# Kernel tuning notes

Measured on AMD Instinct MI355X. Metric: run time of the kernel, lower is better.

The kernel has to match this reference:

```python
import jax, jax.numpy as jnp
import numpy as np

B, T, D, H, L = 32, 512, 256, 512, 3


def setup_inputs() -> dict:
    key = jax.random.key(0)
    ks = jax.random.split(key, 14)
    def lin(k, fan_in, shape):
        return jax.random.normal(k, shape, jnp.float32) / np.sqrt(fan_in)
    inp = {"x": jax.random.normal(ks[0], (B, T, D), jnp.float32)}
    dims_in = [D, H, H]
    i = 1
    for l in range(L):
        inp[f"Wi{l}"] = lin(ks[i + 0], dims_in[l], (3 * H, dims_in[l]))
        inp[f"bi{l}"] = lin(ks[i + 1], dims_in[l], (3 * H,))
        inp[f"Wh{l}"] = lin(ks[i + 2], H, (3 * H, H))
        inp[f"bh{l}"] = lin(ks[i + 3], H, (3 * H,))
        i += 4
    return inp


def _cell(Wi, bi, Wh, bh, xin, h):
    # faithful to ExponentialGatingGRUCell (h2h term appears twice in n preact)
    h2h = h @ Wh.T + bh                      # [B, 3H]
    preact = xin @ Wi.T + bi + h2h           # [B, 3H]
    g = jax.nn.sigmoid(preact[:, : 2 * H])
    r, z = g[:, :H], g[:, H:]
    r = jnp.exp(-jnp.exp(-r))
    z = jnp.exp(-jnp.exp(-z))
    n = jnp.tanh(preact[:, 2 * H:] + r * h2h[:, 2 * H:])
    return (1.0 - z) * n + z * h


def _forward(x, params):
    h0 = tuple(jnp.zeros((x.shape[0], H), x.dtype) for _ in range(L))

    def step(carry, x_t):
        hs = list(carry)
        inp = x_t
        for l in range(L):
            Wi, bi, Wh, bh = params[l]
            hs[l] = _cell(Wi, bi, Wh, bh, inp, hs[l])
            inp = hs[l]
        return tuple(hs), None

    hT, _ = jax.lax.scan(step, h0, jnp.swapaxes(x, 0, 1))  # scan over time
    return hT[-1][:, None, :]  # [B, 1, H]


def reference(x, Wi0, bi0, Wh0, bh0, Wi1, bi1, Wh1, bh1, Wi2, bi2, Wh2, bh2):
    params = [(Wi0, bi0, Wh0, bh0), (Wi1, bi1, Wh1, bh1), (Wi2, bi2, Wh2, bh2)]
    return _forward(x, params)
```

## Files before the change

kernel.cpp:

```cpp
#include <hip/hip_runtime.h>
#include <hip/hip_bf16.h>

typedef __attribute__((ext_vector_type(4))) float fx4;
typedef __attribute__((ext_vector_type(8))) short bf8;
typedef __attribute__((ext_vector_type(4))) short sx4;
typedef __attribute__((ext_vector_type(4))) int ix4;

#define NBLK 96
#define HSZ (32 * 512)

__device__ __forceinline__ short f2bf(float f) {
  __hip_bfloat16 h = __float2bfloat16(f);
  return *reinterpret_cast<short*>(&h);
}
__device__ __forceinline__ float bf2f(short s) {
  union { unsigned u; float f; } c; c.u = ((unsigned)(unsigned short)s) << 16; return c.f;
}
__device__ __forceinline__ float rcpf(float x) { return __builtin_amdgcn_rcpf(x); }
__device__ __forceinline__ bf8 asbf8(ix4 v) { union { ix4 i; bf8 b; } u; u.i = v; return u.b; }

#define LDH(dst, p, OFF) \
  asm volatile("global_load_dwordx4 %0, %1, off offset:" OFF " sc0 sc1" \
               : "=v"(dst) : "v"(p) : "memory")
#define LDP(dst, p, OFF) \
  asm volatile("global_load_dwordx4 %0, %1, off offset:" OFF \
               : "=v"(dst) : "v"(p) : "memory")
#define LD8(OP, A, P) do { \
  OP(A[0], P, "0");   OP(A[1], P, "64");  OP(A[2], P, "128"); OP(A[3], P, "192"); \
  OP(A[4], P, "256"); OP(A[5], P, "320"); OP(A[6], P, "384"); OP(A[7], P, "448"); } while (0)
#define ST4_C(p, v) \
  asm volatile("global_store_dword %0, %1, off sc0 sc1" :: "v"(p), "v"(v) : "memory")
#define LD4_C(d, p) \
  asm volatile("global_load_dword %0, %1, off sc0 sc1\n\ts_waitcnt vmcnt(0)" \
               : "=v"(d) : "v"(p) : "memory")

__global__ __launch_bounds__(256) void conv_x_k(const float* __restrict__ x,
                                                short* __restrict__ xhi, short* __restrict__ xlo) {
  int i = blockIdx.x * 256 + threadIdx.x;
  fx4 v = *(const fx4*)(x + (size_t)i * 4);
  int k = (i * 4) & 255;
  int row = (i * 4) >> 8;
  int b = row >> 9, t = row & 511;
  sx4 hi, lo;
#pragma unroll
  for (int e = 0; e < 4; ++e) {
    hi[e] = f2bf(v[e]);
    lo[e] = f2bf(v[e] - bf2f(hi[e]));
  }
  size_t o = ((size_t)(t * 32 + b)) * 256 + k;
  *(sx4*)(xhi + o) = hi;
  *(sx4*)(xlo + o) = lo;
}

__device__ __forceinline__ void gate_wave(const int* flags, int base, int lane, int need) {
  const int* fp = flags + base + (lane & 31);
  while (true) {
    int v; LD4_C(v, fp);
    if (__ballot(v >= need) == ~0ull) break;
    __builtin_amdgcn_s_sleep(1);
  }
}

template<int L>
__device__ __forceinline__ void rec3_body(
    float (*m_lds)[32][52], float* bias_s,
    const short* __restrict__ xth, const short* __restrict__ xtl,
    const float* __restrict__ Wi, const float* __restrict__ bi,
    const float* __restrict__ Wh, const float* __restrict__ bh,
    short* __restrict__ hgl, const short* __restrict__ hgp,
    int* flags, float* __restrict__ out, int p)
{
  const int tid = threadIdx.x;
  const int j0 = p * 16;
  const int w = tid >> 6, lane = tid & 63, lm = lane & 15, lk = lane >> 4;
  const bool inW = (w < 2);
  constexpr int KIN = (L == 0) ? 256 : 512;

  const int kbase = inW ? ((L == 0) ? 0 : w * 256) : (w - 2) * 256;
  const float* Wf = inW ? Wi : Wh;
  const int wstr = inW ? KIN : 512;

  bf8 bwh[3][8], bwl[3][8];
#pragma unroll
  for (int g = 0; g < 3; ++g) {
    const int grow = g * 512 + j0 + lm;
#pragma unroll
    for (int ks = 0; ks < 8; ++ks) {
      const float* src = Wf + (size_t)grow * wstr + kbase + ks * 32 + lk * 8;
      fx4 f0 = *(const fx4*)(src);
      fx4 f1 = *(const fx4*)(src + 4);
      bf8 vh, vl;
#pragma unroll
      for (int e = 0; e < 4; ++e) {
        vh[e] = f2bf(f0[e]);     vl[e] = f2bf(f0[e] - bf2f(vh[e]));
        vh[4 + e] = f2bf(f1[e]); vl[4 + e] = f2bf(f1[e] - bf2f(vh[4 + e]));
      }
      bwh[g][ks] = vh; bwl[g][ks] = vl;
    }
  }
  if (tid < 48) bias_s[tid] = bi[(tid >> 4) * 512 + j0 + (tid & 15)];
  else if (tid < 96) {
    const int u = tid - 48;
    bias_s[48 + u] = bh[(u >> 4) * 512 + j0 + (u & 15)];
  }
  {
    const int zb = tid >> 3, zc = (tid & 7) * 2;
    ST4_C((int*)(hgl + (size_t)4 * HSZ + (size_t)zb * 512 + j0 + zc), 0);
    ST4_C((int*)(hgl + (size_t)5 * HSZ + (size_t)zb * 512 + j0 + zc), 0);
  }
  asm volatile("s_waitcnt vmcnt(0)" ::: "memory");
  __syncthreads();
  if (tid == 0) ST4_C(flags + L * 32 + p, 2);

  const int cb = tid >> 3, c2 = (tid & 7) * 2;
  float hv0 = 0.f, hv1 = 0.f;
  int bufw = 0;

  for (int s = 0; s < 512; ++s) {
    const int bufr = (bufw == 0) ? 2 : bufw - 1;
    ix4 rh[2][8], rl[2][8];
    if (L == 0 && inW) {
      const short* xh = xth + (size_t)(s * 32 + w * 16 + lm) * 256 + lk * 8;
      const short* xl = xtl + (size_t)(s * 32 + w * 16 + lm) * 256 + lk * 8;
      LD8(LDP, rh[0], xh);
      LD8(LDP, rl[0], xl);
    }

    if (!inW) {
      gate_wave(flags, L * 32, lane, s + 2);
    } else {
      if (L > 0) gate_wave(flags, (L - 1) * 32, lane, s + 3);
      if (L < 2) gate_wave(flags, (L + 1) * 32, lane, s);
    }

    if (inW) {
      if constexpr (L > 0) {
        const short* base = hgp + (size_t)(bufw * 2) * HSZ + (size_t)lm * 512 + kbase + lk * 8;
        LD8(LDH, rh[0], base);
        LD8(LDH, rh[1], base + 16 * 512);
        LD8(LDH, rl[0], base + HSZ);
        LD8(LDH, rl[1], base + HSZ + 16 * 512);
      }
    } else {
      const short* base = hgl + (size_t)(bufr * 2) * HSZ + (size_t)lm * 512 + kbase + lk * 8;
      LD8(LDH, rh[0], base);
      LD8(LDH, rh[1], base + 16 * 512);
      LD8(LDH, rl[0], base + HSZ);
      LD8(LDH, rl[1], base + HSZ + 16 * 512);
    }
    asm volatile("s_waitcnt vmcnt(0)" ::: "memory");
    __builtin_amdgcn_sched_barrier(0);

    fx4 acc[2][3];
#pragma unroll
    for (int mt = 0; mt < 2; ++mt)
#pragma unroll
      for (int g = 0; g < 3; ++g) acc[mt][g] = (fx4){0.f, 0.f, 0.f, 0.f};

    if (L == 0 && inW) {
#pragma unroll
      for (int ks = 0; ks < 8; ++ks) {
        bf8 ah = asbf8(rh[0][ks]);
        bf8 al = asbf8(rl[0][ks]);
#pragma unroll
        for (int g = 0; g < 3; ++g) {
          acc[0][g] = __builtin_amdgcn_mfma_f32_16x16x32_bf16(ah, bwh[g][ks], acc[0][g], 0, 0, 0);
          acc[0][g] = __builtin_amdgcn_mfma_f32_16x16x32_bf16(al, bwh[g][ks], acc[0][g], 0, 0, 0);
          acc[0][g] = __builtin_amdgcn_mfma_f32_16x16x32_bf16(ah, bwl[g][ks], acc[0][g], 0, 0, 0);
        }
      }
    } else {
#pragma unroll
      for (int ks = 0; ks < 8; ++ks) {
#pragma unroll
        for (int mt = 0; mt < 2; ++mt) {
          bf8 ah = asbf8(rh[mt][ks]);
          bf8 al = asbf8(rl[mt][ks]);
#pragma unroll
          for (int g = 0; g < 3; ++g) {
            acc[mt][g] = __builtin_amdgcn_mfma_f32_16x16x32_bf16(ah, bwh[g][ks], acc[mt][g], 0, 0, 0);
            acc[mt][g] = __builtin_amdgcn_mfma_f32_16x16x32_bf16(al, bwh[g][ks], acc[mt][g], 0, 0, 0);
            acc[mt][g] = __builtin_amdgcn_mfma_f32_16x16x32_bf16(ah, bwl[g][ks], acc[mt][g], 0, 0, 0);
          }
        }
      }
    }

    if (L == 0 && inW) {
#pragma unroll
      for (int g = 0; g < 3; ++g)
#pragma unroll
        for (int q = 0; q < 4; ++q)
          m_lds[0][w * 16 + lk * 4 + q][g * 16 + lm] = acc[0][g][q];
    } else {
#pragma unroll
      for (int mt = 0; mt < 2; ++mt)
#pragma unroll
        for (int g = 0; g < 3; ++g)
#pragma unroll
          for (int q = 0; q < 4; ++q)
            m_lds[w][mt * 16 + lk * 4 + q][g * 16 + lm] = acc[mt][g][q];
    }
    __syncthreads();

    float av[3][2], hh[3][2];
#pragma unroll
    for (int g = 0; g < 3; ++g)
#pragma unroll
      for (int e = 0; e < 2; ++e) {
        const int c = g * 16 + c2 + e;
        float ain = m_lds[0][cb][c];
        if (L > 0) ain += m_lds[1][cb][c];
        av[g][e] = ain + bias_s[c];
        hh[g][e] = m_lds[2][cb][c] + m_lds[3][cb][c] + bias_s[48 + c];
      }
    float hvv[2] = {hv0, hv1}, hn[2];
#pragma unroll
    for (int e = 0; e < 2; ++e) {
      float pr = av[0][e] + hh[0][e];
      float pz = av[1][e] + hh[1][e];
      float h2n = hh[2][e];
      float pn = av[2][e] + h2n;
      float sr = rcpf(1.f + __expf(-pr));
      float rr = __expf(-__expf(-sr));
      float sz = rcpf(1.f + __expf(-pz));
      float zz = __expf(-__expf(-sz));
      float na = pn + rr * h2n;
      float ex = __expf(2.f * na);
      float nn = 1.f - 2.f * rcpf(ex + 1.f);
      hn[e] = (1.f - zz) * nn + zz * hvv[e];
    }
    hv0 = hn[0]; hv1 = hn[1];
    short h0h = f2bf(hn[0]), h0l = f2bf(hn[0] - bf2f(h0h));
    short h1h = f2bf(hn[1]), h1l = f2bf(hn[1] - bf2f(h1h));
    int packh = (int)(unsigned short)h0h | ((int)(unsigned short)h1h << 16);
    int packl = (int)(unsigned short)h0l | ((int)(unsigned short)h1l << 16);

    short* hw = hgl + (size_t)(bufw * 2) * HSZ;
    ST4_C((int*)(hw + (size_t)cb * 512 + j0 + c2), packh);
    ST4_C((int*)(hw + HSZ + (size_t)cb * 512 + j0 + c2), packl);
    if (L == 2 && s == 511) {
      out[(size_t)cb * 512 + j0 + c2] = hn[0];
      out[(size_t)cb * 512 + j0 + c2 + 1] = hn[1];
    }
    asm volatile("s_waitcnt vmcnt(0)" ::: "memory");
    __syncthreads();
    if (tid == 0) ST4_C(flags + L * 32 + p, s + 3);

    bufw = (bufw == 2) ? 0 : bufw + 1;
  }
}

__global__ __launch_bounds__(256, 1) void rec3(
    const short* __restrict__ xth, const short* __restrict__ xtl,
    const float* __restrict__ Wi0, const float* __restrict__ bi0,
    const float* __restrict__ Wh0, const float* __restrict__ bh0,
    const float* __restrict__ Wi1, const float* __restrict__ bi1,
    const float* __restrict__ Wh1, const float* __restrict__ bh1,
    const float* __restrict__ Wi2, const float* __restrict__ bi2,
    const float* __restrict__ Wh2, const float* __restrict__ bh2,
    short* __restrict__ hg, int* flags, float* __restrict__ out)
{
  __shared__ __align__(16) float m_lds[4][32][52];
  __shared__ float bias_s[96];
  const int bid = blockIdx.x;
  const int l = bid >> 5, p = bid & 31;
  short* hgl = hg + (size_t)l * 6 * HSZ;
  const short* hgp = (l > 0) ? (hg + (size_t)(l - 1) * 6 * HSZ) : hg;
  if (l == 0)
    rec3_body<0>(m_lds, bias_s, xth, xtl, Wi0, bi0, Wh0, bh0, hgl, hgp, flags, out, p);
  else if (l == 1)
    rec3_body<1>(m_lds, bias_s, nullptr, nullptr, Wi1, bi1, Wh1, bh1, hgl, hgp, flags, out, p);
  else
    rec3_body<2>(m_lds, bias_s, nullptr, nullptr, Wi2, bi2, Wh2, bh2, hgl, hgp, flags, out, p);
}

extern "C" void kernel_launch(void* const* d_in, const int* in_sizes, int n_in,
                              void* d_out, int out_size, void* d_ws, size_t ws_size,
                              hipStream_t stream) {
  const float* x   = (const float*)d_in[0];
  const float* Wi0 = (const float*)d_in[1];
  const float* bi0 = (const float*)d_in[2];
  const float* Wh0 = (const float*)d_in[3];
  const float* bh0 = (const float*)d_in[4];
  const float* Wi1 = (const float*)d_in[5];
  const float* bi1 = (const float*)d_in[6];
  const float* Wh1 = (const float*)d_in[7];
  const float* bh1 = (const float*)d_in[8];
  const float* Wi2 = (const float*)d_in[9];
  const float* bi2 = (const float*)d_in[10];
  const float* Wh2 = (const float*)d_in[11];
  const float* bh2 = (const float*)d_in[12];
  float* out = (float*)d_out;
  (void)in_sizes; (void)n_in; (void)out_size; (void)ws_size;

  char* ws = (char*)d_ws;
  size_t off = 0;
  auto alloc = [&](size_t b) { char* p = ws + off; off = (off + b + 255) & ~(size_t)255; return p; };
  short* xth   = (short*)alloc(16384ull * 256 * 2);
  short* xtl   = (short*)alloc(16384ull * 256 * 2);
  short* hg    = (short*)alloc(3ull * 6 * HSZ * 2);
  int*   flags = (int*)alloc(NBLK * 4);

  hipMemsetAsync(flags, 0, NBLK * 4, stream);
  hipLaunchKernelGGL(conv_x_k, dim3(4096), dim3(256), 0, stream, x, xth, xtl);
  hipLaunchKernelGGL(rec3, dim3(NBLK), dim3(256), 0, stream,
                     xth, xtl,
                     Wi0, bi0, Wh0, bh0,
                     Wi1, bi1, Wh1, bh1,
                     Wi2, bi2, Wh2, bh2,
                     hg, flags, out);
}
```

Measured before the change: 3.829 ms.

## Replace flag-based inter-block sync with sentinel-polled per-timestep hidden-state planes

```diff
diff --git a/kernel.cpp b/kernel.cpp
--- a/kernel.cpp
+++ b/kernel.cpp
@@ -8,6 +8,7 @@
 
 #define NBLK 96
 #define HSZ (32 * 512)
+#define NPLANE 513
 
 __device__ __forceinline__ short f2bf(float f) {
   __hip_bfloat16 h = __float2bfloat16(f);
@@ -30,9 +31,9 @@
   OP(A[4], P, "256"); OP(A[5], P, "320"); OP(A[6], P, "384"); OP(A[7], P, "448"); } while (0)
 #define ST4_C(p, v) \
   asm volatile("global_store_dword %0, %1, off sc0 sc1" :: "v"(p), "v"(v) : "memory")
-#define LD4_C(d, p) \
-  asm volatile("global_load_dword %0, %1, off sc0 sc1\n\ts_waitcnt vmcnt(0)" \
-               : "=v"(d) : "v"(p) : "memory")
+#define LBAR() do { \
+  asm volatile("s_waitcnt lgkmcnt(0)" ::: "memory"); \
+  __builtin_amdgcn_s_barrier(); } while (0)
 
 __global__ __launch_bounds__(256) void conv_x_k(const float* __restrict__ x,
                                                 short* __restrict__ xhi, short* __restrict__ xlo) {
@@ -52,13 +53,26 @@
   *(sx4*)(xlo + o) = lo;
 }
 
-__device__ __forceinline__ void gate_wave(const int* flags, int base, int lane, int need) {
-  const int* fp = flags + base + (lane & 31);
+__device__ __forceinline__ void poll_h(ix4 (&rh)[2][8], ix4 (&rl)[2][8], const short* base) {
   while (true) {
-    int v; LD4_C(v, fp);
-    if (__ballot(v >= need) == ~0ull) break;
+    LD8(LDH, rh[0], base);
+    LD8(LDH, rh[1], base + 16 * 512);
+    LD8(LDH, rl[0], base + HSZ);
+    LD8(LDH, rl[1], base + HSZ + 16 * 512);
+    asm volatile("s_waitcnt vmcnt(0)" ::: "memory");
+    __builtin_amdgcn_sched_barrier(0);
+    int bad = 0;
+#pragma unroll
+    for (int mt = 0; mt < 2; ++mt)
+#pragma unroll
+      for (int k = 0; k < 8; ++k)
+#pragma unroll
+        for (int e = 0; e < 4; ++e)
+          bad |= (rh[mt][k][e] == -1) | (rl[mt][k][e] == -1);
+    if (__ballot(bad != 0) == 0) break;
     __builtin_amdgcn_s_sleep(1);
   }
+  __builtin_amdgcn_sched_barrier(0);
 }
 
 template<int L>
@@ -68,7 +82,7 @@
     const float* __restrict__ Wi, const float* __restrict__ bi,
     const float* __restrict__ Wh, const float* __restrict__ bh,
     short* __restrict__ hgl, const short* __restrict__ hgp,
-    int* flags, float* __restrict__ out, int p)
+    float* __restrict__ out, int p)
 {
   const int tid = threadIdx.x;
   const int j0 = p * 16;
@@ -105,51 +119,29 @@
   }
   {
     const int zb = tid >> 3, zc = (tid & 7) * 2;
-    ST4_C((int*)(hgl + (size_t)4 * HSZ + (size_t)zb * 512 + j0 + zc), 0);
-    ST4_C((int*)(hgl + (size_t)5 * HSZ + (size_t)zb * 512 + j0 + zc), 0);
-  }
-  asm volatile("s_waitcnt vmcnt(0)" ::: "memory");
-  __syncthreads();
-  if (tid == 0) ST4_C(flags + L * 32 + p, 2);
+    ST4_C((int*)(hgl + (size_t)zb * 512 + j0 + zc), 0);
+    ST4_C((int*)(hgl + HSZ + (size_t)zb * 512 + j0 + zc), 0);
+  }
 
   const int cb = tid >> 3, c2 = (tid & 7) * 2;
   float hv0 = 0.f, hv1 = 0.f;
-  int bufw = 0;
 
   for (int s = 0; s < 512; ++s) {
-    const int bufr = (bufw == 0) ? 2 : bufw - 1;
     ix4 rh[2][8], rl[2][8];
     if (L == 0 && inW) {
       const short* xh = xth + (size_t)(s * 32 + w * 16 + lm) * 256 + lk * 8;
       const short* xl = xtl + (size_t)(s * 32 + w * 16 + lm) * 256 + lk * 8;
       LD8(LDP, rh[0], xh);
       LD8(LDP, rl[0], xl);
-    }
-
-    if (!inW) {
-      gate_wave(flags, L * 32, lane, s + 2);
+      asm volatile("s_waitcnt vmcnt(0)" ::: "memory");
+      __builtin_amdgcn_sched_barrier(0);
+    } else if (inW) {
+      const short* base = hgp + (size_t)(s + 1) * 2 * HSZ + (size_t)lm * 512 + kbase + lk * 8;
+      poll_h(rh, rl, base);
     } else {
-      if (L > 0) gate_wave(flags, (L - 1) * 32, lane, s + 3);
-      if (L < 2) gate_wave(flags, (L + 1) * 32, lane, s);
-    }
-
-    if (inW) {
-      if constexpr (L > 0) {
-        const short* base = hgp + (size_t)(bufw * 2) * HSZ + (size_t)lm * 512 + kbase + lk * 8;
-        LD8(LDH, rh[0], base);
-        LD8(LDH, rh[1], base + 16 * 512);
-        LD8(LDH, rl[0], base + HSZ);
-        LD8(LDH, rl[1], base + HSZ + 16 * 512);
-      }
-    } else {
-      const short* base = hgl + (size_t)(bufr * 2) * HSZ + (size_t)lm * 512 + kbase + lk * 8;
-      LD8(LDH, rh[0], base);
-      LD8(LDH, rh[1], base + 16 * 512);
-      LD8(LDH, rl[0], base + HSZ);
-      LD8(LDH, rl[1], base + HSZ + 16 * 512);
-    }
-    asm volatile("s_waitcnt vmcnt(0)" ::: "memory");
-    __builtin_amdgcn_sched_barrier(0);
+      const short* base = hgl + (size_t)s * 2 * HSZ + (size_t)lm * 512 + kbase + lk * 8;
+      poll_h(rh, rl, base);
+    }
 
     fx4 acc[2][3];
 #pragma unroll
@@ -201,7 +193,7 @@
           for (int q = 0; q < 4; ++q)
             m_lds[w][mt * 16 + lk * 4 + q][g * 16 + lm] = acc[mt][g][q];
     }
-    __syncthreads();
+    LBAR();
 
     float av[3][2], hh[3][2];
 #pragma unroll
@@ -236,18 +228,14 @@
     int packh = (int)(unsigned short)h0h | ((int)(unsigned short)h1h << 16);
     int packl = (int)(unsigned short)h0l | ((int)(unsigned short)h1l << 16);
 
-    short* hw = hgl + (size_t)(bufw * 2) * HSZ;
+    short* hw = hgl + (size_t)(s + 1) * 2 * HSZ;
     ST4_C((int*)(hw + (size_t)cb * 512 + j0 + c2), packh);
     ST4_C((int*)(hw + HSZ + (size_t)cb * 512 + j0 + c2), packl);
     if (L == 2 && s == 511) {
       out[(size_t)cb * 512 + j0 + c2] = hn[0];
       out[(size_t)cb * 512 + j0 + c2 + 1] = hn[1];
     }
-    asm volatile("s_waitcnt vmcnt(0)" ::: "memory");
-    __syncthreads();
-    if (tid == 0) ST4_C(flags + L * 32 + p, s + 3);
-
-    bufw = (bufw == 2) ? 0 : bufw + 1;
+    LBAR();
   }
 }
 
@@ -259,20 +247,20 @@
     const float* __restrict__ Wh1, const float* __restrict__ bh1,
     const float* __restrict__ Wi2, const float* __restrict__ bi2,
     const float* __restrict__ Wh2, const float* __restrict__ bh2,
-    short* __restrict__ hg, int* flags, float* __restrict__ out)
+    short* __restrict__ hg, float* __restrict__ out)
 {
   __shared__ __align__(16) float m_lds[4][32][52];
   __shared__ float bias_s[96];
   const int bid = blockIdx.x;
   const int l = bid >> 5, p = bid & 31;
-  short* hgl = hg + (size_t)l * 6 * HSZ;
-  const short* hgp = (l > 0) ? (hg + (size_t)(l - 1) * 6 * HSZ) : hg;
+  short* hgl = hg + (size_t)l * NPLANE * 2 * HSZ;
+  const short* hgp = (l > 0) ? (hg + (size_t)(l - 1) * NPLANE * 2 * HSZ) : hg;
   if (l == 0)
-    rec3_body<0>(m_lds, bias_s, xth, xtl, Wi0, bi0, Wh0, bh0, hgl, hgp, flags, out, p);
+    rec3_body<0>(m_lds, bias_s, xth, xtl, Wi0, bi0, Wh0, bh0, hgl, hgp, out, p);
   else if (l == 1)
-    rec3_body<1>(m_lds, bias_s, nullptr, nullptr, Wi1, bi1, Wh1, bh1, hgl, hgp, flags, out, p);
+    rec3_body<1>(m_lds, bias_s, nullptr, nullptr, Wi1, bi1, Wh1, bh1, hgl, hgp, out, p);
   else
-    rec3_body<2>(m_lds, bias_s, nullptr, nullptr, Wi2, bi2, Wh2, bh2, hgl, hgp, flags, out, p);
+    rec3_body<2>(m_lds, bias_s, nullptr, nullptr, Wi2, bi2, Wh2, bh2, hgl, hgp, out, p);
 }
 
 extern "C" void kernel_launch(void* const* d_in, const int* in_sizes, int n_in,
@@ -297,17 +285,17 @@
   char* ws = (char*)d_ws;
   size_t off = 0;
   auto alloc = [&](size_t b) { char* p = ws + off; off = (off + b + 255) & ~(size_t)255; return p; };
-  short* xth   = (short*)alloc(16384ull * 256 * 2);
-  short* xtl   = (short*)alloc(16384ull * 256 * 2);
-  short* hg    = (short*)alloc(3ull * 6 * HSZ * 2);
-  int*   flags = (int*)alloc(NBLK * 4);
-
-  hipMemsetAsync(flags, 0, NBLK * 4, stream);
+  short* xth = (short*)alloc(16384ull * 256 * 2);
+  short* xtl = (short*)alloc(16384ull * 256 * 2);
+  const size_t hbytes = 3ull * NPLANE * 2 * HSZ * 2;
+  short* hg  = (short*)alloc(hbytes);
+
+  hipMemsetAsync(hg, 0xFF, hbytes, stream);
   hipLaunchKernelGGL(conv_x_k, dim3(4096), dim3(256), 0, stream, x, xth, xtl);
   hipLaunchKernelGGL(rec3, dim3(NBLK), dim3(256), 0, stream,
                      xth, xtl,
                      Wi0, bi0, Wh0, bh0,
                      Wi1, bi1, Wh1, bh1,
                      Wi2, bi2, Wh2, bh2,
-                     hg, flags, out);
-}
+                     hg, out);
+}
```

Measured after the change: 4.201 ms. 9.7% more time.
